# Performance work log

Hardware: AMD Instinct MI355X
Metric: run time of the kernel (lower is better)

## Reference

```python
import jax, jax.numpy as jnp
import numpy as np

H, HKV, D, HID = 16, 8, 128, 2048   # heads, kv heads, head_dim, hidden
TOTAL, NSEG = 2048, 4               # packed tokens, number of sequences
SEG = TOTAL // NSEG
EPS = 1e-6


def setup_inputs() -> dict:
    key = jax.random.key(0)
    ks = jax.random.split(key, 8)
    x = jax.random.normal(ks[0], (1, TOTAL, HID), jnp.float32)
    # RoPE tables, positions restart at each packed segment
    inv_freq = 1.0 / (10000.0 ** (jnp.arange(0, D, 2, dtype=jnp.float32) / D))
    pos = jnp.tile(jnp.arange(SEG, dtype=jnp.float32), NSEG)  # [TOTAL]
    ang = pos[:, None] * inv_freq[None, :]                    # [TOTAL, D/2]
    emb = jnp.concatenate([ang, ang], axis=-1)                # [TOTAL, D]
    cos, sin = jnp.cos(emb), jnp.sin(emb)
    std = 0.02
    Wq = jax.random.normal(ks[1], (H * D, HID), jnp.float32) * std
    Wk = jax.random.normal(ks[2], (HKV * D, HID), jnp.float32) * std
    Wv = jax.random.normal(ks[3], (HKV * D, HID), jnp.float32) * std
    Wo = jax.random.normal(ks[4], (HID, H * D), jnp.float32) * std
    q_norm_w = jnp.ones((D,), jnp.float32)
    k_norm_w = jnp.ones((D,), jnp.float32)
    cu_seqlens = (jnp.arange(NSEG + 1, dtype=jnp.int32) * SEG)
    return {
        'x': x, 'cos': cos, 'sin': sin,
        'cu_seqlens': cu_seqlens, 'max_seqlen': SEG,
        'Wq': Wq, 'Wk': Wk, 'Wv': Wv, 'Wo': Wo,
        'q_norm_w': q_norm_w, 'k_norm_w': k_norm_w,
    }


def _rms(x, w):
    xf = x.astype(jnp.float32)
    var = jnp.mean(xf * xf, axis=-1, keepdims=True)
    return (w * xf * jax.lax.rsqrt(var + EPS)).astype(x.dtype)


def _rotate_half(x):
    x1, x2 = jnp.split(x, 2, axis=-1)
    return jnp.concatenate([-x2, x1], axis=-1)


def reference(x, cos, sin, cu_seqlens, max_seqlen, Wq, Wk, Wv, Wo, q_norm_w, k_norm_w):
    total = x.shape[1]
    xt = x[0]                                   # [total, HID]
    q = (xt @ Wq.T).reshape(total, H, D)
    k = (xt @ Wk.T).reshape(total, HKV, D)
    v = (xt @ Wv.T).reshape(total, HKV, D)
    q = _rms(q, q_norm_w)
    k = _rms(k, k_norm_w)
    c = cos[:, None, :]                          # [total, 1, D]
    s = sin[:, None, :]
    q = q * c + _rotate_half(q) * s
    k = k * c + _rotate_half(k) * s
    # GQA: repeat kv heads
    n_rep = H // HKV
    k = jnp.repeat(k, n_rep, axis=1)             # [total, H, D]
    v = jnp.repeat(v, n_rep, axis=1)
    # varlen causal mask (block-diagonal causal from cu_seqlens)
    idx = jnp.arange(total)
    seg = jnp.searchsorted(cu_seqlens[1:], idx, side='right')
    mask = (seg[:, None] == seg[None, :]) & (idx[:, None] >= idx[None, :])
    scale = 1.0 / jnp.sqrt(jnp.float32(D))
    scores = jnp.einsum('qhd,khd->hqk', q, k) * scale
    scores = jnp.where(mask[None, :, :], scores, -jnp.inf)
    probs = jax.nn.softmax(scores, axis=-1)
    out = jnp.einsum('hqk,khd->qhd', probs, v).reshape(1, total, H * D)
    return out @ Wo.T
```

## Files before the change

### kernel.cpp

```cpp
#include <hip/hip_runtime.h>
#include <hip/hip_bf16.h>
#include <stdint.h>

#define TOTAL 2048
#define NSEG  4
#define SEG   512
#define NH    16
#define NKV   8
#define DH    128
#define HID   2048
#define QKV_N 4096

typedef __attribute__((ext_vector_type(8))) __bf16 bf16x8;
typedef __attribute__((ext_vector_type(8))) unsigned short u16x8;
typedef __attribute__((ext_vector_type(4))) float f32x4;

__device__ __forceinline__ unsigned short f2bf(float f) {
  unsigned int u = __float_as_uint(f);
  u += 0x7fffu + ((u >> 16) & 1u);
  return (unsigned short)(u >> 16);
}

__device__ __forceinline__ void gll16(const void* g, void* l) {
  __builtin_amdgcn_global_load_lds(
      (const __attribute__((address_space(1))) void*)(uintptr_t)g,
      (__attribute__((address_space(3))) void*)(uint32_t)(uintptr_t)l,
      16, 0, 0);
}

__global__ __launch_bounds__(256) void cvt_all(const float* __restrict__ x,
                                               const float* __restrict__ wq,
                                               const float* __restrict__ wk,
                                               const float* __restrict__ wv,
                                               const float* __restrict__ wo,
                                               unsigned short* __restrict__ xb,
                                               unsigned short* __restrict__ wqkvb,
                                               unsigned short* __restrict__ wob) {
  const int N0 = 1048576, N1 = 1048576, N2 = 524288, N3 = 524288;
  int i = blockIdx.x * 256 + threadIdx.x;
  #pragma unroll
  for (int it = 0; it < 4; ++it, i += 1048576) {
    const float* src; unsigned short* dst; int j = i;
    if (j < N0)              { src = x;  dst = xb; }
    else if ((j -= N0) < N1) { src = wq; dst = wqkvb; }
    else if ((j -= N1) < N2) { src = wk; dst = wqkvb + 4194304; }
    else if ((j -= N2) < N3) { src = wv; dst = wqkvb + 6291456; }
    else                     { j -= N3; src = wo; dst = wob; }
    float4 v = reinterpret_cast<const float4*>(src)[j];
    ushort4 o;
    o.x = f2bf(v.x); o.y = f2bf(v.y); o.z = f2bf(v.z); o.w = f2bf(v.w);
    reinterpret_cast<ushort4*>(dst)[j] = o;
  }
}

__global__ __launch_bounds__(256) void gemm_bt(const unsigned short* __restrict__ A,
                                               const unsigned short* __restrict__ B,
                                               float* __restrict__ C,
                                               int M, int N, int K) {
  __shared__ unsigned short As[2][128 * 64];
  __shared__ unsigned short Bs[2][128 * 64];
  const int t    = threadIdx.x;
  const int lane = t & 63;
  const int w    = t >> 6;
  const int wr   = (w >> 1) * 64;
  const int wc   = (w & 1) * 64;
  const long row0 = (long)blockIdx.y * 128;
  const long col0 = (long)blockIdx.x * 128;

  const int lrow  = lane >> 3;
  const int gslot = (lane & 7) ^ (lrow & 7);
  const unsigned short* gA[4];
  const unsigned short* gB[4];
  #pragma unroll
  for (int j = 0; j < 4; ++j) {
    const int c = w * 4 + j;
    gA[j] = A + (row0 + c * 8 + lrow) * (long)K + gslot * 8;
    gB[j] = B + (col0 + c * 8 + lrow) * (long)K + gslot * 8;
  }

  const int fr = lane & 15;
  const int l4 = lane >> 4;

  f32x4 acc[4][4];
  #pragma unroll
  for (int m = 0; m < 4; ++m)
    #pragma unroll
    for (int n = 0; n < 4; ++n) acc[m][n] = (f32x4){0.f, 0.f, 0.f, 0.f};

  #pragma unroll
  for (int j = 0; j < 4; ++j) {
    gll16(gA[j], &As[0][(w * 4 + j) * 512]);
    gll16(gB[j], &Bs[0][(w * 4 + j) * 512]);
  }
  __syncthreads();

  int cur = 0;
  for (int k0 = 0; k0 < K; k0 += 64) {
    if (k0 + 64 < K) {
      #pragma unroll
      for (int j = 0; j < 4; ++j) {
        gll16(gA[j] + k0 + 64, &As[cur ^ 1][(w * 4 + j) * 512]);
        gll16(gB[j] + k0 + 64, &Bs[cur ^ 1][(w * 4 + j) * 512]);
      }
    }

    #pragma unroll
    for (int kk = 0; kk < 2; ++kk) {
      bf16x8 af[4], bfv[4];
      #pragma unroll
      for (int m = 0; m < 4; ++m) {
        const int ra = wr + m * 16 + fr;
        af[m] = *reinterpret_cast<const bf16x8*>(
            &As[cur][ra * 64 + (((kk * 4 + l4) ^ (ra & 7)) * 8)]);
      }
      #pragma unroll
      for (int n = 0; n < 4; ++n) {
        const int rb = wc + n * 16 + fr;
        bfv[n] = *reinterpret_cast<const bf16x8*>(
            &Bs[cur][rb * 64 + (((kk * 4 + l4) ^ (rb & 7)) * 8)]);
      }
      #pragma unroll
      for (int m = 0; m < 4; ++m)
        #pragma unroll
        for (int n = 0; n < 4; ++n)
          acc[m][n] = __builtin_amdgcn_mfma_f32_16x16x32_bf16(af[m], bfv[n], acc[m][n], 0, 0, 0);
    }

    __syncthreads();
    cur ^= 1;
  }

  const int crow = (lane >> 4) * 4;
  const int ccol = lane & 15;
  #pragma unroll
  for (int m = 0; m < 4; ++m)
    #pragma unroll
    for (int n = 0; n < 4; ++n)
      #pragma unroll
      for (int r = 0; r < 4; ++r)
        C[(row0 + wr + m * 16 + crow + r) * (long)N + col0 + wc + n * 16 + ccol] =
            acc[m][n][r];
}

__global__ __launch_bounds__(256) void norm_rope(const float* __restrict__ Cqkv,
                                                 const float* __restrict__ cosb,
                                                 const float* __restrict__ sinb,
                                                 const float* __restrict__ qw,
                                                 const float* __restrict__ kw,
                                                 unsigned short* __restrict__ qb2,
                                                 unsigned short* __restrict__ ktb) {
  const int lane = threadIdx.x & 63;
  const int t  = blockIdx.x * 4 + (threadIdx.x >> 6);
  const int hs = blockIdx.y;

  const float* row = Cqkv + (size_t)t * QKV_N + hs * DH;
  float a = row[lane];
  float b = row[lane + 64];

  float ss = a * a + b * b;
  #pragma unroll
  for (int off = 32; off; off >>= 1) ss += __shfl_xor(ss, off, 64);
  float r = rsqrtf(ss * (1.0f / 128.0f) + 1e-6f);
  const float* wgt = (hs < 16) ? qw : kw;
  a = a * r * wgt[lane];
  b = b * r * wgt[lane + 64];
  float c0 = cosb[t * DH + lane],      c1 = cosb[t * DH + lane + 64];
  float s0 = sinb[t * DH + lane],      s1 = sinb[t * DH + lane + 64];
  float o0 = a * c0 - b * s0;
  float o1 = b * c1 + a * s1;

  unsigned short* dst = (hs < 16)
      ? qb2 + ((size_t)hs * TOTAL + t) * DH
      : ktb + ((size_t)(hs - 16) * TOTAL + t) * DH;
  dst[lane]      = f2bf(o0);
  dst[lane + 64] = f2bf(o1);
}

__global__ __launch_bounds__(256) void vt_kernel(const float* __restrict__ Cqkv,
                                                 unsigned short* __restrict__ vtb) {
  __shared__ unsigned short tile[64][132];
  const int tid = threadIdx.x;
  const int t0  = blockIdx.x * 64;
  const int hkv = blockIdx.y;
  const float* src = Cqkv + (size_t)t0 * QKV_N + (NH + NKV) * DH + hkv * DH;
  #pragma unroll
  for (int it = 0; it < 8; ++it) {
    const int i   = it * 256 + tid;
    const int row = i >> 5;
    const int c4  = i & 31;
    float4 v = *reinterpret_cast<const float4*>(src + (size_t)row * QKV_N + c4 * 4);
    ushort4 o;
    o.x = f2bf(v.x); o.y = f2bf(v.y); o.z = f2bf(v.z); o.w = f2bf(v.w);
    *reinterpret_cast<ushort4*>(&tile[row][c4 * 4]) = o;
  }
  __syncthreads();
  #pragma unroll
  for (int it = 0; it < 4; ++it) {
    const int i  = it * 256 + tid;
    const int d  = i >> 3;
    const int tc = i & 7;
    u16x8 o;
    #pragma unroll
    for (int j = 0; j < 8; ++j) o[j] = tile[tc * 8 + j][d];
    *reinterpret_cast<u16x8*>(vtb + ((size_t)hkv * DH + d) * TOTAL + t0 + tc * 8) = o;
  }
}

__global__ __launch_bounds__(256) void attn_mfma(const unsigned short* __restrict__ qb2,
                                                 const unsigned short* __restrict__ ktb,
                                                 const unsigned short* __restrict__ vtb,
                                                 unsigned short* __restrict__ aob) {
  __shared__ unsigned short Ks[2][64 * 128];
  __shared__ unsigned short Vt[2][128 * 64];
  __shared__ unsigned short ps[4][16][72];

  const int tid  = threadIdx.x;
  const int lane = tid & 63;
  const int w    = tid >> 6;
  const int b    = blockIdx.x;
  const int qt   = 7 - (b & 7);
  const int h    = (b >> 3) & 15;
  const int seg  = b >> 7;
  const int hkv  = h >> 1;
  const int q0   = seg * SEG + qt * 64;
  const int l15  = lane & 15;
  const int l4   = lane >> 4;

  const unsigned short* qptr = qb2 + ((size_t)h * TOTAL + q0 + w * 16 + l15) * DH + l4 * 8;
  bf16x8 aq[4];
  #pragma unroll
  for (int ks = 0; ks < 4; ++ks)
    aq[ks] = *reinterpret_cast<const bf16x8*>(qptr + ks * 32);

  const unsigned short* kbase = ktb + (size_t)hkv * TOTAL * DH;
  const unsigned short* vbase = vtb + (size_t)hkv * DH * TOTAL;

  int ksrc[4], vsrc[4], ldst[4];
  #pragma unroll
  for (int j = 0; j < 4; ++j) {
    const int cc = w * 4 + j;
    const int kr = cc * 4 + (lane >> 4);
    ksrc[j] = kr * DH + (((lane & 15) ^ (kr & 7)) * 8);
    const int vd = cc * 8 + (lane >> 3);
    vsrc[j] = vd * TOTAL + (((lane & 7) ^ (vd & 7)) * 8);
    ldst[j] = cc * 512;
  }

  f32x4 acc[8];
  #pragma unroll
  for (int n = 0; n < 8; ++n) acc[n] = (f32x4){0.f, 0.f, 0.f, 0.f};
  float m_r[4] = {-1e30f, -1e30f, -1e30f, -1e30f};
  float l_r[4] = {0.f, 0.f, 0.f, 0.f};

  const float scale = 0.08838834764831845f;
  const int kvS = seg * SEG;

  #pragma unroll
  for (int j = 0; j < 4; ++j) {
    gll16(kbase + (size_t)kvS * DH + ksrc[j], &Ks[0][ldst[j]]);
    gll16(vbase + kvS + vsrc[j], &Vt[0][ldst[j]]);
  }
  __syncthreads();

  int cur = 0;
  for (int kt = 0; kt <= qt; ++kt) {
    const int kv0 = kvS + kt * 64;
    if (kt < qt) {
      #pragma unroll
      for (int j = 0; j < 4; ++j) {
        gll16(kbase + (size_t)(kv0 + 64) * DH + ksrc[j], &Ks[cur ^ 1][ldst[j]]);
        gll16(vbase + (kv0 + 64) + vsrc[j], &Vt[cur ^ 1][ldst[j]]);
      }
    }

    const bool diag = (kt == qt);

    f32x4 sv[4];
    #pragma unroll
    for (int c = 0; c < 4; ++c) {
      if (diag && c * 16 > w * 16 + 15) {
        sv[c] = (f32x4){-1e30f, -1e30f, -1e30f, -1e30f};
      } else {
        f32x4 s = (f32x4){0.f, 0.f, 0.f, 0.f};
        const int kr = c * 16 + l15;
        #pragma unroll
        for (int ks = 0; ks < 4; ++ks) {
          const int byte = (kr << 8) + (((ks * 32 + l4 * 8) * 2) ^ ((kr & 7) << 4));
          bf16x8 bk = *reinterpret_cast<const bf16x8*>((const char*)Ks[cur] + byte);
          s = __builtin_amdgcn_mfma_f32_16x16x32_bf16(aq[ks], bk, s, 0, 0, 0);
        }
        sv[c] = s;
      }
    }

    float p[4][4];
    #pragma unroll
    for (int r = 0; r < 4; ++r) {
      const int qq = w * 16 + l4 * 4 + r;
      float mx = -1e30f;
      #pragma unroll
      for (int c = 0; c < 4; ++c) {
        float s = sv[c][r] * scale;
        if (diag) {
          const int kk = c * 16 + l15;
          if (kk > qq) s = -1e30f;
        }
        p[c][r] = s;
        mx = fmaxf(mx, s);
      }
      #pragma unroll
      for (int off = 1; off < 16; off <<= 1) mx = fmaxf(mx, __shfl_xor(mx, off));
      const float nm = fmaxf(m_r[r], mx);
      const float f  = __expf(m_r[r] - nm);
      m_r[r] = nm;
      float ls = 0.f;
      #pragma unroll
      for (int c = 0; c < 4; ++c) { p[c][r] = __expf(p[c][r] - nm); ls += p[c][r]; }
      #pragma unroll
      for (int off = 1; off < 16; off <<= 1) ls += __shfl_xor(ls, off);
      l_r[r] = l_r[r] * f + ls;
      #pragma unroll
      for (int n = 0; n < 8; ++n) acc[n][r] *= f;
    }

    #pragma unroll
    for (int c = 0; c < 4; ++c)
      #pragma unroll
      for (int r = 0; r < 4; ++r)
        ps[w][l4 * 4 + r][c * 16 + l15] = f2bf(p[c][r]);

    #pragma unroll
    for (int ks2 = 0; ks2 < 2; ++ks2) {
      if (diag && ks2 * 32 > w * 16 + 15) continue;
      bf16x8 pa = *reinterpret_cast<const bf16x8*>(&ps[w][l15][ks2 * 32 + l4 * 8]);
      #pragma unroll
      for (int n = 0; n < 8; ++n) {
        const int d = n * 16 + l15;
        const int byte = (d << 7) + (((ks2 * 32 + l4 * 8) * 2) ^ ((d & 7) << 4));
        bf16x8 bv = *reinterpret_cast<const bf16x8*>((const char*)Vt[cur] + byte);
        acc[n] = __builtin_amdgcn_mfma_f32_16x16x32_bf16(pa, bv, acc[n], 0, 0, 0);
      }
    }

    __syncthreads();
    cur ^= 1;
  }

  #pragma unroll
  for (int r = 0; r < 4; ++r) {
    const float inv = 1.0f / l_r[r];
    unsigned short* orow = aob + ((size_t)(q0 + w * 16 + l4 * 4 + r) * NH + h) * DH;
    #pragma unroll
    for (int n = 0; n < 8; ++n)
      orow[n * 16 + l15] = f2bf(acc[n][r] * inv);
  }
}

extern "C" void kernel_launch(void* const* d_in, const int* in_sizes, int n_in,
                              void* d_out, int out_size, void* d_ws, size_t ws_size,
                              hipStream_t stream) {
  const float* x    = (const float*)d_in[0];
  const float* cosb = (const float*)d_in[1];
  const float* sinb = (const float*)d_in[2];
  const float* Wq   = (const float*)d_in[5];
  const float* Wk   = (const float*)d_in[6];
  const float* Wv   = (const float*)d_in[7];
  const float* Wo   = (const float*)d_in[8];
  const float* qw   = (const float*)d_in[9];
  const float* kw   = (const float*)d_in[10];
  float* out = (float*)d_out;

  char* ws = (char*)d_ws;
  unsigned short* xb    = (unsigned short*)(ws + 0);
  unsigned short* Wqkvb = (unsigned short*)(ws + (8u  << 20));
  unsigned short* Wob   = (unsigned short*)(ws + (24u << 20));
  float*          Cqkv  = (float*)         (ws + (32u << 20));
  unsigned short* qb2   = (unsigned short*)(ws + (64u << 20));
  unsigned short* ktb   = (unsigned short*)(ws + (72u << 20));
  unsigned short* vtb   = (unsigned short*)(ws + (76u << 20));
  unsigned short* aob   = (unsigned short*)(ws + (80u << 20));

  cvt_all<<<4096, 256, 0, stream>>>(x, Wq, Wk, Wv, Wo, xb, Wqkvb, Wob);

  {
    dim3 g(QKV_N / 128, TOTAL / 128);
    gemm_bt<<<g, 256, 0, stream>>>(xb, Wqkvb, Cqkv, TOTAL, QKV_N, HID);
  }

  {
    dim3 g(TOTAL / 4, 24);
    norm_rope<<<g, 256, 0, stream>>>(Cqkv, cosb, sinb, qw, kw, qb2, ktb);
  }
  {
    dim3 g(TOTAL / 64, NKV);
    vt_kernel<<<g, 256, 0, stream>>>(Cqkv, vtb);
  }

  attn_mfma<<<NSEG * NH * 8, 256, 0, stream>>>(qb2, ktb, vtb, aob);

  {
    dim3 g(HID / 128, TOTAL / 128);
    gemm_bt<<<g, 256, 0, stream>>>(aob, Wob, out, TOTAL, HID, HID);
  }
}
```

Measured before the change: 121.1 us.

## Retile GEMM to 64x128 blocks with two waves and 32-wide K steps

Changes the GEMM kernel from 128x128 tiles with four waves and K-step 64 to 64x128 tiles with two waves and K-step 32, with a new 4-slot LDS swizzle and load mapping. The grid doubles in the M direction, so more blocks can spread across the many CUs of the device and each block uses less LDS. The cost is lower arithmetic intensity per block, more K iterations and barriers, and more redundant global reads of B.

```diff
diff --git a/kernel.cpp b/kernel.cpp
--- a/kernel.cpp
+++ b/kernel.cpp
@@ -53,29 +53,35 @@
   }
 }
 
-__global__ __launch_bounds__(256) void gemm_bt(const unsigned short* __restrict__ A,
+__global__ __launch_bounds__(128) void gemm_bt(const unsigned short* __restrict__ A,
                                                const unsigned short* __restrict__ B,
                                                float* __restrict__ C,
                                                int M, int N, int K) {
-  __shared__ unsigned short As[2][128 * 64];
-  __shared__ unsigned short Bs[2][128 * 64];
+  __shared__ unsigned short As[2][64 * 32];
+  __shared__ unsigned short Bs[2][128 * 32];
   const int t    = threadIdx.x;
   const int lane = t & 63;
   const int w    = t >> 6;
-  const int wr   = (w >> 1) * 64;
-  const int wc   = (w & 1) * 64;
-  const long row0 = (long)blockIdx.y * 128;
+  const int wc   = w * 64;
+  const long row0 = (long)blockIdx.y * 64;
   const long col0 = (long)blockIdx.x * 128;
 
-  const int lrow  = lane >> 3;
-  const int gslot = (lane & 7) ^ (lrow & 7);
-  const unsigned short* gA[4];
+  const int lr = lane >> 2;
+  const int ls = lane & 3;
+  const unsigned short* gA[2];
   const unsigned short* gB[4];
+  int ldA[2], ldB[4];
+  #pragma unroll
+  for (int j = 0; j < 2; ++j) {
+    const int row = (w * 2 + j) * 16 + lr;
+    gA[j] = A + (row0 + row) * (long)K + ((ls ^ (row & 3)) * 8);
+    ldA[j] = (w * 2 + j) * 512;
+  }
   #pragma unroll
   for (int j = 0; j < 4; ++j) {
-    const int c = w * 4 + j;
-    gA[j] = A + (row0 + c * 8 + lrow) * (long)K + gslot * 8;
-    gB[j] = B + (col0 + c * 8 + lrow) * (long)K + gslot * 8;
+    const int row = (w * 4 + j) * 16 + lr;
+    gB[j] = B + (col0 + row) * (long)K + ((ls ^ (row & 3)) * 8);
+    ldB[j] = (w * 4 + j) * 512;
   }
 
   const int fr = lane & 15;
@@ -88,43 +94,38 @@
     for (int n = 0; n < 4; ++n) acc[m][n] = (f32x4){0.f, 0.f, 0.f, 0.f};
 
   #pragma unroll
-  for (int j = 0; j < 4; ++j) {
-    gll16(gA[j], &As[0][(w * 4 + j) * 512]);
-    gll16(gB[j], &Bs[0][(w * 4 + j) * 512]);
-  }
+  for (int j = 0; j < 2; ++j) gll16(gA[j], &As[0][ldA[j]]);
+  #pragma unroll
+  for (int j = 0; j < 4; ++j) gll16(gB[j], &Bs[0][ldB[j]]);
   __syncthreads();
 
   int cur = 0;
-  for (int k0 = 0; k0 < K; k0 += 64) {
-    if (k0 + 64 < K) {
-      #pragma unroll
-      for (int j = 0; j < 4; ++j) {
-        gll16(gA[j] + k0 + 64, &As[cur ^ 1][(w * 4 + j) * 512]);
-        gll16(gB[j] + k0 + 64, &Bs[cur ^ 1][(w * 4 + j) * 512]);
-      }
-    }
-
-    #pragma unroll
-    for (int kk = 0; kk < 2; ++kk) {
-      bf16x8 af[4], bfv[4];
-      #pragma unroll
-      for (int m = 0; m < 4; ++m) {
-        const int ra = wr + m * 16 + fr;
-        af[m] = *reinterpret_cast<const bf16x8*>(
-            &As[cur][ra * 64 + (((kk * 4 + l4) ^ (ra & 7)) * 8)]);
-      }
-      #pragma unroll
-      for (int n = 0; n < 4; ++n) {
-        const int rb = wc + n * 16 + fr;
-        bfv[n] = *reinterpret_cast<const bf16x8*>(
-            &Bs[cur][rb * 64 + (((kk * 4 + l4) ^ (rb & 7)) * 8)]);
-      }
-      #pragma unroll
-      for (int m = 0; m < 4; ++m)
-        #pragma unroll
-        for (int n = 0; n < 4; ++n)
-          acc[m][n] = __builtin_amdgcn_mfma_f32_16x16x32_bf16(af[m], bfv[n], acc[m][n], 0, 0, 0);
-    }
+  for (int k0 = 0; k0 < K; k0 += 32) {
+    if (k0 + 32 < K) {
+      #pragma unroll
+      for (int j = 0; j < 2; ++j) gll16(gA[j] + k0 + 32, &As[cur ^ 1][ldA[j]]);
+      #pragma unroll
+      for (int j = 0; j < 4; ++j) gll16(gB[j] + k0 + 32, &Bs[cur ^ 1][ldB[j]]);
+    }
+
+    bf16x8 af[4], bfv[4];
+    #pragma unroll
+    for (int m = 0; m < 4; ++m) {
+      const int ra = m * 16 + fr;
+      af[m] = *reinterpret_cast<const bf16x8*>(
+          &As[cur][ra * 32 + ((l4 ^ (ra & 3)) * 8)]);
+    }
+    #pragma unroll
+    for (int n = 0; n < 4; ++n) {
+      const int rb = wc + n * 16 + fr;
+      bfv[n] = *reinterpret_cast<const bf16x8*>(
+          &Bs[cur][rb * 32 + ((l4 ^ (rb & 3)) * 8)]);
+    }
+    #pragma unroll
+    for (int m = 0; m < 4; ++m)
+      #pragma unroll
+      for (int n = 0; n < 4; ++n)
+        acc[m][n] = __builtin_amdgcn_mfma_f32_16x16x32_bf16(af[m], bfv[n], acc[m][n], 0, 0, 0);
 
     __syncthreads();
     cur ^= 1;
@@ -138,7 +139,7 @@
     for (int n = 0; n < 4; ++n)
       #pragma unroll
       for (int r = 0; r < 4; ++r)
-        C[(row0 + wr + m * 16 + crow + r) * (long)N + col0 + wc + n * 16 + ccol] =
+        C[(row0 + m * 16 + crow + r) * (long)N + col0 + wc + n * 16 + ccol] =
             acc[m][n][r];
 }
 
@@ -383,8 +384,8 @@
   cvt_all<<<4096, 256, 0, stream>>>(x, Wq, Wk, Wv, Wo, xb, Wqkvb, Wob);
 
   {
-    dim3 g(QKV_N / 128, TOTAL / 128);
-    gemm_bt<<<g, 256, 0, stream>>>(xb, Wqkvb, Cqkv, TOTAL, QKV_N, HID);
+    dim3 g(QKV_N / 128, TOTAL / 64);
+    gemm_bt<<<g, 128, 0, stream>>>(xb, Wqkvb, Cqkv, TOTAL, QKV_N, HID);
   }
 
   {
@@ -399,7 +400,7 @@
   attn_mfma<<<NSEG * NH * 8, 256, 0, stream>>>(qb2, ktb, vtb, aob);
 
   {
-    dim3 g(HID / 128, TOTAL / 128);
-    gemm_bt<<<g, 256, 0, stream>>>(aob, Wob, out, TOTAL, HID, HID);
-  }
-}
+    dim3 g(HID / 128, TOTAL / 64);
+    gemm_bt<<<g, 128, 0, stream>>>(aob, Wob, out, TOTAL, HID, HID);
+  }
+}
```

After: 147.7 us. +21.9%, slower.

## Triple-buffer GEMM LDS tiles with partial vmcnt waits and a single barrier

Applied to the files above, without the earlier changes.

The bf16 GEMM moves from double to triple buffering of its LDS tiles. It prefetches two k-tiles ahead and uses an explicit s_waitcnt vmcnt(8) so only the oldest tile must have landed. Each iteration now needs one barrier instead of two __syncthreads. The goal is to hide global-to-LDS load latency better. In exchange LDS use rises to 96KB per block, which may reduce occupancy, and correctness now depends on the hand-counted vmcnt.

```diff
diff --git a/kernel.cpp b/kernel.cpp
--- a/kernel.cpp
+++ b/kernel.cpp
@@ -57,8 +57,8 @@
                                                const unsigned short* __restrict__ B,
                                                float* __restrict__ C,
                                                int M, int N, int K) {
-  __shared__ unsigned short As[2][128 * 64];
-  __shared__ unsigned short Bs[2][128 * 64];
+  __shared__ unsigned short As[3][128 * 64];
+  __shared__ unsigned short Bs[3][128 * 64];
   const int t    = threadIdx.x;
   const int lane = t & 63;
   const int w    = t >> 6;
@@ -71,11 +71,13 @@
   const int gslot = (lane & 7) ^ (lrow & 7);
   const unsigned short* gA[4];
   const unsigned short* gB[4];
+  int loff[4];
   #pragma unroll
   for (int j = 0; j < 4; ++j) {
     const int c = w * 4 + j;
     gA[j] = A + (row0 + c * 8 + lrow) * (long)K + gslot * 8;
     gB[j] = B + (col0 + c * 8 + lrow) * (long)K + gslot * 8;
+    loff[j] = c * 512;
   }
 
   const int fr = lane & 15;
@@ -89,18 +91,28 @@
 
   #pragma unroll
   for (int j = 0; j < 4; ++j) {
-    gll16(gA[j], &As[0][(w * 4 + j) * 512]);
-    gll16(gB[j], &Bs[0][(w * 4 + j) * 512]);
-  }
-  __syncthreads();
-
-  int cur = 0;
+    gll16(gA[j], &As[0][loff[j]]);
+    gll16(gB[j], &Bs[0][loff[j]]);
+  }
+  #pragma unroll
+  for (int j = 0; j < 4; ++j) {
+    gll16(gA[j] + 64, &As[1][loff[j]]);
+    gll16(gB[j] + 64, &Bs[1][loff[j]]);
+  }
+
+  unsigned short *Ac = As[0], *An = As[1], *Af = As[2];
+  unsigned short *Bc = Bs[0], *Bn = Bs[1], *Bf = Bs[2];
+
   for (int k0 = 0; k0 < K; k0 += 64) {
-    if (k0 + 64 < K) {
+    if (k0 + 64 < K) asm volatile("s_waitcnt vmcnt(8)" ::: "memory");
+    else             asm volatile("s_waitcnt vmcnt(0)" ::: "memory");
+    __builtin_amdgcn_s_barrier();
+
+    if (k0 + 128 < K) {
       #pragma unroll
       for (int j = 0; j < 4; ++j) {
-        gll16(gA[j] + k0 + 64, &As[cur ^ 1][(w * 4 + j) * 512]);
-        gll16(gB[j] + k0 + 64, &Bs[cur ^ 1][(w * 4 + j) * 512]);
+        gll16(gA[j] + k0 + 128, &Af[loff[j]]);
+        gll16(gB[j] + k0 + 128, &Bf[loff[j]]);
       }
     }
 
@@ -111,13 +123,13 @@
       for (int m = 0; m < 4; ++m) {
         const int ra = wr + m * 16 + fr;
         af[m] = *reinterpret_cast<const bf16x8*>(
-            &As[cur][ra * 64 + (((kk * 4 + l4) ^ (ra & 7)) * 8)]);
+            &Ac[ra * 64 + (((kk * 4 + l4) ^ (ra & 7)) * 8)]);
       }
       #pragma unroll
       for (int n = 0; n < 4; ++n) {
         const int rb = wc + n * 16 + fr;
         bfv[n] = *reinterpret_cast<const bf16x8*>(
-            &Bs[cur][rb * 64 + (((kk * 4 + l4) ^ (rb & 7)) * 8)]);
+            &Bc[rb * 64 + (((kk * 4 + l4) ^ (rb & 7)) * 8)]);
       }
       #pragma unroll
       for (int m = 0; m < 4; ++m)
@@ -126,8 +138,8 @@
           acc[m][n] = __builtin_amdgcn_mfma_f32_16x16x32_bf16(af[m], bfv[n], acc[m][n], 0, 0, 0);
     }
 
-    __syncthreads();
-    cur ^= 1;
+    unsigned short* ta = Ac; Ac = An; An = Af; Af = ta;
+    unsigned short* tb = Bc; Bc = Bn; Bn = Bf; Bf = tb;
   }
 
   const int crow = (lane >> 4) * 4;
```

New measurement: 132.6 us. +9.4%, slower.

## Use partial vmcnt waits for true double buffering and smaller tiles for output GEMM

Applied to the files above, without the earlier changes.

The __syncthreads after issuing the next tile's global-to-LDS loads is replaced by explicit s_waitcnt vmcnt(N) plus raw barriers. Only the current tile's loads must complete, so the prefetch of the next tile can overlap the MFMA work in both the GEMM and attention kernels. The GEMM is templated on BM, and the output projection uses 64-row tiles with 128 threads so twice as many blocks fill the CUs. The hand-counted vmcnt values depend on the exact load counts per wave, so a miscount would silently race.

```diff
diff --git a/kernel.cpp b/kernel.cpp
--- a/kernel.cpp
+++ b/kernel.cpp
@@ -27,6 +27,7 @@
       (__attribute__((address_space(3))) void*)(uint32_t)(uintptr_t)l,
       16, 0, 0);
 }
+__device__ __forceinline__ void cfence() { asm volatile("" ::: "memory"); }
 
 __global__ __launch_bounds__(256) void cvt_all(const float* __restrict__ x,
                                                const float* __restrict__ wq,
@@ -53,29 +54,39 @@
   }
 }
 
-__global__ __launch_bounds__(256) void gemm_bt(const unsigned short* __restrict__ A,
-                                               const unsigned short* __restrict__ B,
-                                               float* __restrict__ C,
-                                               int M, int N, int K) {
-  __shared__ unsigned short As[2][128 * 64];
+template<int BM>
+__global__ __launch_bounds__(BM == 128 ? 256 : 128)
+void gemm_bt(const unsigned short* __restrict__ A,
+             const unsigned short* __restrict__ B,
+             float* __restrict__ C, int M, int N, int K) {
+  constexpr int NW  = (BM == 128) ? 4 : 2;
+  constexpr int APW = (BM / 8) / NW;
+  constexpr int BPW = 16 / NW;
+  __shared__ unsigned short As[2][BM * 64];
   __shared__ unsigned short Bs[2][128 * 64];
   const int t    = threadIdx.x;
   const int lane = t & 63;
   const int w    = t >> 6;
-  const int wr   = (w >> 1) * 64;
-  const int wc   = (w & 1) * 64;
-  const long row0 = (long)blockIdx.y * 128;
+  const int wr   = (BM == 128) ? (w >> 1) * 64 : 0;
+  const int wc   = (BM == 128) ? (w & 1) * 64 : w * 64;
+  const long row0 = (long)blockIdx.y * BM;
   const long col0 = (long)blockIdx.x * 128;
 
   const int lrow  = lane >> 3;
   const int gslot = (lane & 7) ^ (lrow & 7);
-  const unsigned short* gA[4];
-  const unsigned short* gB[4];
-  #pragma unroll
-  for (int j = 0; j < 4; ++j) {
-    const int c = w * 4 + j;
+  const unsigned short* gA[APW]; int lA[APW];
+  const unsigned short* gB[BPW]; int lB[BPW];
+  #pragma unroll
+  for (int j = 0; j < APW; ++j) {
+    const int c = w * APW + j;
     gA[j] = A + (row0 + c * 8 + lrow) * (long)K + gslot * 8;
+    lA[j] = c * 512;
+  }
+  #pragma unroll
+  for (int j = 0; j < BPW; ++j) {
+    const int c = w * BPW + j;
     gB[j] = B + (col0 + c * 8 + lrow) * (long)K + gslot * 8;
+    lB[j] = c * 512;
   }
 
   const int fr = lane & 15;
@@ -88,21 +99,27 @@
     for (int n = 0; n < 4; ++n) acc[m][n] = (f32x4){0.f, 0.f, 0.f, 0.f};
 
   #pragma unroll
-  for (int j = 0; j < 4; ++j) {
-    gll16(gA[j], &As[0][(w * 4 + j) * 512]);
-    gll16(gB[j], &Bs[0][(w * 4 + j) * 512]);
-  }
-  __syncthreads();
+  for (int j = 0; j < APW; ++j) gll16(gA[j], &As[0][lA[j]]);
+  #pragma unroll
+  for (int j = 0; j < BPW; ++j) gll16(gB[j], &Bs[0][lB[j]]);
+  asm volatile("s_waitcnt vmcnt(0)" ::: "memory");
+  __builtin_amdgcn_s_barrier();
+  cfence();
 
   int cur = 0;
   for (int k0 = 0; k0 < K; k0 += 64) {
     if (k0 + 64 < K) {
       #pragma unroll
-      for (int j = 0; j < 4; ++j) {
-        gll16(gA[j] + k0 + 64, &As[cur ^ 1][(w * 4 + j) * 512]);
-        gll16(gB[j] + k0 + 64, &Bs[cur ^ 1][(w * 4 + j) * 512]);
-      }
-    }
+      for (int j = 0; j < APW; ++j) gll16(gA[j] + k0 + 64, &As[cur ^ 1][lA[j]]);
+      #pragma unroll
+      for (int j = 0; j < BPW; ++j) gll16(gB[j] + k0 + 64, &Bs[cur ^ 1][lB[j]]);
+      if constexpr (BM == 128) asm volatile("s_waitcnt vmcnt(8)" ::: "memory");
+      else                     asm volatile("s_waitcnt vmcnt(12)" ::: "memory");
+    } else {
+      asm volatile("s_waitcnt vmcnt(0)" ::: "memory");
+    }
+    __builtin_amdgcn_s_barrier();
+    cfence();
 
     #pragma unroll
     for (int kk = 0; kk < 2; ++kk) {
@@ -126,7 +143,9 @@
           acc[m][n] = __builtin_amdgcn_mfma_f32_16x16x32_bf16(af[m], bfv[n], acc[m][n], 0, 0, 0);
     }
 
-    __syncthreads();
+    cfence();
+    __builtin_amdgcn_s_barrier();
+    cfence();
     cur ^= 1;
   }
 
@@ -260,7 +279,9 @@
     gll16(kbase + (size_t)kvS * DH + ksrc[j], &Ks[0][ldst[j]]);
     gll16(vbase + kvS + vsrc[j], &Vt[0][ldst[j]]);
   }
-  __syncthreads();
+  asm volatile("s_waitcnt vmcnt(0)" ::: "memory");
+  __builtin_amdgcn_s_barrier();
+  cfence();
 
   int cur = 0;
   for (int kt = 0; kt <= qt; ++kt) {
@@ -271,7 +292,12 @@
         gll16(kbase + (size_t)(kv0 + 64) * DH + ksrc[j], &Ks[cur ^ 1][ldst[j]]);
         gll16(vbase + (kv0 + 64) + vsrc[j], &Vt[cur ^ 1][ldst[j]]);
       }
-    }
+      asm volatile("s_waitcnt vmcnt(8)" ::: "memory");
+    } else {
+      asm volatile("s_waitcnt vmcnt(0)" ::: "memory");
+    }
+    __builtin_amdgcn_s_barrier();
+    cfence();
 
     const bool diag = (kt == qt);
 
@@ -342,7 +368,9 @@
       }
     }
 
-    __syncthreads();
+    cfence();
+    __builtin_amdgcn_s_barrier();
+    cfence();
     cur ^= 1;
   }
 
@@ -384,7 +412,7 @@
 
   {
     dim3 g(QKV_N / 128, TOTAL / 128);
-    gemm_bt<<<g, 256, 0, stream>>>(xb, Wqkvb, Cqkv, TOTAL, QKV_N, HID);
+    gemm_bt<128><<<g, 256, 0, stream>>>(xb, Wqkvb, Cqkv, TOTAL, QKV_N, HID);
   }
 
   {
@@ -399,7 +427,7 @@
   attn_mfma<<<NSEG * NH * 8, 256, 0, stream>>>(qb2, ktb, vtb, aob);
 
   {
-    dim3 g(HID / 128, TOTAL / 128);
-    gemm_bt<<<g, 256, 0, stream>>>(aob, Wob, out, TOTAL, HID, HID);
-  }
-}
+    dim3 g(HID / 128, TOTAL / 64);
+    gemm_bt<64><<<g, 128, 0, stream>>>(aob, Wob, out, TOTAL, HID, HID);
+  }
+}
```

Result: no change. 122.7 us (+1.3%).
